# Performance work log

Hardware: AMD Instinct MI355X
Metric: run time of the kernel (lower is better)

Reference implementation:

```python
import jax, jax.numpy as jnp
import numpy as np

B, N, D, H, DK, DV = 16, 512, 512, 8, 64, 64


def setup_inputs() -> dict:
    key = jax.random.key(0)
    ks = jax.random.split(key, 16)
    xav = lambda k, fi, fo: jax.random.uniform(k, (fi, fo), jnp.float32,
                                               -jnp.sqrt(6.0 / (fi + fo)), jnp.sqrt(6.0 / (fi + fo)))
    return {
        "queries": jax.random.normal(ks[0], (B, N, D), jnp.float32),
        "keys": jax.random.normal(ks[1], (B, N, D), jnp.float32),
        "values": jax.random.normal(ks[2], (B, N, D), jnp.float32),
        "box_relation_embed_matrix": jax.random.uniform(ks[3], (B, H, N, N), jnp.float32),
        "ExtrAtt": jax.random.normal(ks[4], (B, H, N, N), jnp.float32),
        "Wq": xav(ks[5], D, H * DK), "bq": jnp.zeros((H * DK,), jnp.float32),
        "Wk": xav(ks[6], D, H * DK), "bk": jnp.zeros((H * DK,), jnp.float32),
        "Wv": xav(ks[7], D, H * DV), "bv": jnp.zeros((H * DV,), jnp.float32),
        "Wo": xav(ks[8], H * DV, D), "bo": jnp.zeros((D,), jnp.float32),
    }


def reference(queries, keys, values, box_relation_embed_matrix, ExtrAtt,
              Wq, bq, Wk, bk, Wv, bv, Wo, bo):
    b_s, nq, _ = queries.shape
    nk = keys.shape[1]
    # projections -> [B, H, N, d]
    q = (queries @ Wq + bq).reshape(b_s, nq, H, DK).transpose(0, 2, 1, 3)
    k = (keys @ Wk + bk).reshape(b_s, nk, H, DK).transpose(0, 2, 1, 3)
    v = (values @ Wv + bv).reshape(b_s, nk, H, DV).transpose(0, 2, 1, 3)
    scale = 1.0 / jnp.sqrt(jnp.asarray(DK, queries.dtype))
    att = jnp.einsum('bhqd,bhkd->bhqk', q, k) * scale
    # log geometric (box) bias + content attention, first softmax
    w_mn = jnp.log(jnp.clip(box_relation_embed_matrix, 1e-6, None)) + att
    w_mn = jax.nn.softmax(w_mn, axis=-1)
    # dropout is identity in eval; add extra attention and re-normalize
    att2 = jax.nn.softmax(w_mn + ExtrAtt, axis=-1)
    out = jnp.einsum('bhqk,bhkd->bhqd', att2, v)
    out = out.transpose(0, 2, 1, 3).reshape(b_s, nq, H * DV)
    return out @ Wo + bo
```

## Files before the change

kernel.cpp:

```cpp
#include <hip/hip_runtime.h>
#include <hip/hip_bf16.h>

#define NB 16
#define NN 512
#define ND 512
#define NH 8

using short8 = __attribute__((ext_vector_type(8))) short;
using f32x4  = __attribute__((ext_vector_type(4))) float;

static __device__ __forceinline__ unsigned short f2bf(float f) {
  unsigned u = __builtin_bit_cast(unsigned, f);
  unsigned r = 0x7fffu + ((u >> 16) & 1u);
  return (unsigned short)((u + r) >> 16);
}

__global__ __launch_bounds__(256) void wprep(
    const float* __restrict__ Wq, const float* __restrict__ Wk,
    const float* __restrict__ Wv, const float* __restrict__ Wo,
    unsigned short* __restrict__ T) {
  const float* W;
  switch (blockIdx.z) {
    case 0: W = Wq; break;
    case 1: W = Wk; break;
    case 2: W = Wv; break;
    default: W = Wo; break;
  }
  unsigned short* Wt = T + (size_t)blockIdx.z * 512 * 512;
  __shared__ float tile[64][65];
  const int t = threadIdx.x;
  const int k0 = blockIdx.x * 64, n0 = blockIdx.y * 64;
#pragma unroll
  for (int it = 0; it < 4; ++it) {
    int row = it * 16 + (t >> 4);
    int c4 = (t & 15) * 4;
    float4 v = *(const float4*)&W[(size_t)(k0 + row) * 512 + n0 + c4];
    tile[row][c4] = v.x; tile[row][c4 + 1] = v.y;
    tile[row][c4 + 2] = v.z; tile[row][c4 + 3] = v.w;
  }
  __syncthreads();
#pragma unroll
  for (int it = 0; it < 4; ++it) {
    int nr = it * 16 + (t >> 4);
    int k4 = (t & 15) * 4;
    ushort4 o;
    o.x = f2bf(tile[k4 + 0][nr]); o.y = f2bf(tile[k4 + 1][nr]);
    o.z = f2bf(tile[k4 + 2][nr]); o.w = f2bf(tile[k4 + 3][nr]);
    *(ushort4*)&Wt[(size_t)(n0 + nr) * 512 + k0 + k4] = o;
  }
}

__global__ __launch_bounds__(256) void qkv_gemm(
    const float* __restrict__ Xq, const float* __restrict__ Xk,
    const float* __restrict__ Xv, const unsigned short* __restrict__ Wt,
    const float* __restrict__ bq, const float* __restrict__ bk,
    const float* __restrict__ bv, unsigned short* __restrict__ q_ws,
    unsigned short* __restrict__ k_ws, unsigned short* __restrict__ vt_ws) {
  const int zi = blockIdx.z;
  const float* X = (zi == 0) ? Xq : (zi == 1) ? Xk : Xv;
  const unsigned short* Wz = Wt + (size_t)zi * 512 * 512;
  const float* bias = (zi == 0) ? bq : (zi == 1) ? bk : bv;
  const int m0 = blockIdx.x * 128, n0 = blockIdx.y * 128;
  __shared__ unsigned short Al[2][128][40];
  __shared__ unsigned short Bl[2][128][40];
  const int t = threadIdx.x;
  const int w = t >> 6, l = t & 63;
  const int lr = l & 15, lg = l >> 4;
  const int wr = (w >> 1) * 64, wc = (w & 1) * 64;
  f32x4 acc[4][4] = {};
  for (int kk = 0; kk < 512; kk += 64) {
    __syncthreads();
    {
      const int colk = (t & 15) * 4;
      const int kc = colk >> 5, kin = colk & 31;
#pragma unroll
      for (int p = 0; p < 8; ++p) {
        int row = p * 16 + (t >> 4);
        float4 v = *(const float4*)&X[(size_t)(m0 + row) * 512 + kk + colk];
        ushort4 o;
        o.x = f2bf(v.x); o.y = f2bf(v.y); o.z = f2bf(v.z); o.w = f2bf(v.w);
        *(ushort4*)&Al[kc][row][kin] = o;
      }
      const int colk8 = (t & 7) * 8;
      const int kc2 = colk8 >> 5, kin2 = colk8 & 31;
#pragma unroll
      for (int p = 0; p < 4; ++p) {
        int row = p * 32 + (t >> 3);
        short8 v = *(const short8*)&Wz[(size_t)(n0 + row) * 512 + kk + colk8];
        *(short8*)&Bl[kc2][row][kin2] = v;
      }
    }
    __syncthreads();
#pragma unroll
    for (int kc = 0; kc < 2; ++kc) {
      short8 a[4], b[4];
      const int lk = lg * 8;
#pragma unroll
      for (int i = 0; i < 4; ++i) a[i] = *(const short8*)&Al[kc][wr + i * 16 + lr][lk];
#pragma unroll
      for (int i = 0; i < 4; ++i) b[i] = *(const short8*)&Bl[kc][wc + i * 16 + lr][lk];
#pragma unroll
      for (int i = 0; i < 4; ++i)
#pragma unroll
        for (int j = 0; j < 4; ++j)
          acc[i][j] = __builtin_amdgcn_mfma_f32_16x16x32_bf16(a[i], b[j], acc[i][j], 0, 0, 0);
    }
  }
#pragma unroll
  for (int j = 0; j < 4; ++j) {
    const int col = n0 + wc + j * 16 + lr;
    const float bb = bias[col];
    const int hh = col >> 6, dv = col & 63;
#pragma unroll
    for (int i = 0; i < 4; ++i) {
      const int mbase = m0 + wr + i * 16 + lg * 4;
      const int b_ = mbase >> 9, nt = mbase & 511;
      if (zi == 2) {
        ushort4 o;
        o.x = f2bf(acc[i][j][0] + bb); o.y = f2bf(acc[i][j][1] + bb);
        o.z = f2bf(acc[i][j][2] + bb); o.w = f2bf(acc[i][j][3] + bb);
        *(ushort4*)&vt_ws[((size_t)(b_ * NH + hh) * 64 + dv) * 512 + nt] = o;
      } else {
        unsigned short* dst = (zi == 0) ? q_ws : k_ws;
#pragma unroll
        for (int r = 0; r < 4; ++r)
          dst[((size_t)(b_ * NH + hh) * 512 + nt + r) * 64 + dv] = f2bf(acc[i][j][r] + bb);
      }
    }
  }
}

__global__ __launch_bounds__(256, 3) void attn_kernel(
    const unsigned short* __restrict__ q_ws, const unsigned short* __restrict__ k_ws,
    const unsigned short* __restrict__ vt_ws, const float* __restrict__ box,
    const float* __restrict__ Ext, unsigned short* __restrict__ hidden) {
  const int t = threadIdx.x;
  const int w = t >> 6, l = t & 63;
  const int lr = l & 15, lg = l >> 4;
  const int bh = blockIdx.y;
  const int q0 = blockIdx.x * 32;
  const int b = bh >> 3, h = bh & 7;

  const unsigned short* Qp = q_ws + (size_t)bh * 512 * 64;
  const unsigned short* Kp = k_ws + (size_t)bh * 512 * 64;
  const unsigned short* Vt = vt_ws + (size_t)bh * 64 * 512;
  const float* boxp = box + ((size_t)bh * 512 + q0) * 512;
  const float* Ep = Ext + ((size_t)bh * 512 + q0) * 512;

  __shared__ float red[4][32];
  __shared__ float red2[4][32];
  __shared__ __align__(16) unsigned char wsh[4][9216];

  const int n0w = w * 128;

  f32x4 bx[2][8];
#pragma unroll
  for (int c = 0; c < 8; ++c) {
    const int cb = n0w + c * 16 + lg * 4;
    bx[0][c] = *(const f32x4*)&boxp[(size_t)lr * 512 + cb];
    bx[1][c] = *(const f32x4*)&boxp[(size_t)(16 + lr) * 512 + cb];
  }
  __builtin_amdgcn_sched_barrier(0);

  short8 qf[2][2];
#pragma unroll
  for (int rg = 0; rg < 2; ++rg)
#pragma unroll
    for (int kc = 0; kc < 2; ++kc)
      qf[rg][kc] = *(const short8*)&Qp[(size_t)(q0 + rg * 16 + lr) * 64 + kc * 32 + lg * 8];

  f32x4 z[2][8];
  float s1a = 0.f, s1b = 0.f;
#pragma unroll
  for (int c = 0; c < 8; ++c) {
    const int krow = n0w + c * 16 + lr;
    short8 kf0 = *(const short8*)&Kp[(size_t)krow * 64 + lg * 8];
    short8 kf1 = *(const short8*)&Kp[(size_t)krow * 64 + 32 + lg * 8];
    f32x4 a0 = {0.f, 0.f, 0.f, 0.f}, a1 = {0.f, 0.f, 0.f, 0.f};
    a0 = __builtin_amdgcn_mfma_f32_16x16x32_bf16(kf0, qf[0][0], a0, 0, 0, 0);
    a0 = __builtin_amdgcn_mfma_f32_16x16x32_bf16(kf1, qf[0][1], a0, 0, 0, 0);
    a1 = __builtin_amdgcn_mfma_f32_16x16x32_bf16(kf0, qf[1][0], a1, 0, 0, 0);
    a1 = __builtin_amdgcn_mfma_f32_16x16x32_bf16(kf1, qf[1][1], a1, 0, 0, 0);
#pragma unroll
    for (int r = 0; r < 4; ++r) {
      float e0 = __expf(a0[r] * 0.125f + __logf(fmaxf(bx[0][c][r], 1e-6f)));
      float e1 = __expf(a1[r] * 0.125f + __logf(fmaxf(bx[1][c][r], 1e-6f)));
      z[0][c][r] = e0; s1a += e0;
      z[1][c][r] = e1; s1b += e1;
    }
  }
  s1a += __shfl_xor(s1a, 16); s1a += __shfl_xor(s1a, 32);
  s1b += __shfl_xor(s1b, 16); s1b += __shfl_xor(s1b, 32);
  if (lg == 0) {
    red[w][lr] = s1a;
    red[w][16 + lr] = s1b;
  }
  f32x4 ex[2][8];
#pragma unroll
  for (int c = 0; c < 8; ++c) {
    const int cb = n0w + c * 16 + lg * 4;
    ex[0][c] = *(const f32x4*)&Ep[(size_t)lr * 512 + cb];
    ex[1][c] = *(const f32x4*)&Ep[(size_t)(16 + lr) * 512 + cb];
  }
  __builtin_amdgcn_sched_barrier(0);
  __syncthreads();
  float l1i[2];
#pragma unroll
  for (int rg = 0; rg < 2; ++rg) {
    const int lrow = rg * 16 + lr;
    l1i[rg] = 1.0f / (red[0][lrow] + red[1][lrow] + red[2][lrow] + red[3][lrow]);
  }
  float s2a = 0.f, s2b = 0.f;
#pragma unroll
  for (int c = 0; c < 8; ++c)
#pragma unroll
    for (int r = 0; r < 4; ++r) {
      float e0 = __expf(z[0][c][r] * l1i[0] + ex[0][c][r]);
      float e1 = __expf(z[1][c][r] * l1i[1] + ex[1][c][r]);
      z[0][c][r] = e0; s2a += e0;
      z[1][c][r] = e1; s2b += e1;
    }
  s2a += __shfl_xor(s2a, 16); s2a += __shfl_xor(s2a, 32);
  s2b += __shfl_xor(s2b, 16); s2b += __shfl_xor(s2b, 32);
  if (lg == 0) {
    red2[w][lr] = s2a;
    red2[w][16 + lr] = s2b;
  }
  __syncthreads();
  float l2i[2];
#pragma unroll
  for (int rg = 0; rg < 2; ++rg) {
    const int lrow = rg * 16 + lr;
    l2i[rg] = 1.0f / (red2[0][lrow] + red2[1][lrow] + red2[2][lrow] + red2[3][lrow]);
  }
  unsigned short(*Pw)[144] = (unsigned short(*)[144])wsh[w];
#pragma unroll
  for (int rg = 0; rg < 2; ++rg)
#pragma unroll
    for (int c = 0; c < 8; ++c) {
      ushort4 o;
      o.x = f2bf(z[rg][c][0] * l2i[rg]);
      o.y = f2bf(z[rg][c][1] * l2i[rg]);
      o.z = f2bf(z[rg][c][2] * l2i[rg]);
      o.w = f2bf(z[rg][c][3] * l2i[rg]);
      *(ushort4*)&Pw[rg * 16 + lr][c * 16 + lg * 4] = o;
    }
  f32x4 o[2][4] = {};
#pragma unroll
  for (int kc = 0; kc < 4; ++kc) {
    short8 pa0 = *(const short8*)&Pw[lr][kc * 32 + lg * 8];
    short8 pa1 = *(const short8*)&Pw[16 + lr][kc * 32 + lg * 8];
#pragma unroll
    for (int c2 = 0; c2 < 4; ++c2) {
      short8 vf = *(const short8*)&Vt[(size_t)(c2 * 16 + lr) * 512 + n0w + kc * 32 + lg * 8];
      o[0][c2] = __builtin_amdgcn_mfma_f32_16x16x32_bf16(pa0, vf, o[0][c2], 0, 0, 0);
      o[1][c2] = __builtin_amdgcn_mfma_f32_16x16x32_bf16(pa1, vf, o[1][c2], 0, 0, 0);
    }
  }
  float* ow = (float*)wsh[w];
#pragma unroll
  for (int rg = 0; rg < 2; ++rg)
#pragma unroll
    for (int c2 = 0; c2 < 4; ++c2)
#pragma unroll
      for (int r = 0; r < 4; ++r)
        ow[(rg * 16 + lg * 4 + r) * 68 + c2 * 16 + lr] = o[rg][c2][r];
  __syncthreads();
#pragma unroll
  for (int i = 0; i < 2; ++i) {
    const int lrow = i * 16 + (t >> 4);
    const int d4 = (t & 15) * 4;
    f32x4 s = *(const f32x4*)&((const float*)wsh[0])[lrow * 68 + d4];
#pragma unroll
    for (int w2 = 1; w2 < 4; ++w2) {
      f32x4 p = *(const f32x4*)&((const float*)wsh[w2])[lrow * 68 + d4];
#pragma unroll
      for (int r = 0; r < 4; ++r) s[r] += p[r];
    }
    ushort4 oo;
    oo.x = f2bf(s[0]); oo.y = f2bf(s[1]); oo.z = f2bf(s[2]); oo.w = f2bf(s[3]);
    *(ushort4*)&hidden[(size_t)(b * 512 + q0 + lrow) * 512 + h * 64 + d4] = oo;
  }
}

__global__ __launch_bounds__(256) void out_gemm(
    const unsigned short* __restrict__ hidden, const unsigned short* __restrict__ WoT,
    const float* __restrict__ bo, float* __restrict__ out) {
  const int m0 = blockIdx.x * 128, n0 = blockIdx.y * 128;
  __shared__ unsigned short Al[2][128][40];
  __shared__ unsigned short Bl[2][128][40];
  const int t = threadIdx.x;
  const int w = t >> 6, l = t & 63;
  const int lr = l & 15, lg = l >> 4;
  const int wr = (w >> 1) * 64, wc = (w & 1) * 64;
  f32x4 acc[4][4] = {};
  for (int kk = 0; kk < 512; kk += 64) {
    __syncthreads();
    {
      const int colk8 = (t & 7) * 8;
      const int kc2 = colk8 >> 5, kin2 = colk8 & 31;
#pragma unroll
      for (int p = 0; p < 4; ++p) {
        int row = p * 32 + (t >> 3);
        short8 v = *(const short8*)&hidden[(size_t)(m0 + row) * 512 + kk + colk8];
        *(short8*)&Al[kc2][row][kin2] = v;
      }
#pragma unroll
      for (int p = 0; p < 4; ++p) {
        int row = p * 32 + (t >> 3);
        short8 v = *(const short8*)&WoT[(size_t)(n0 + row) * 512 + kk + colk8];
        *(short8*)&Bl[kc2][row][kin2] = v;
      }
    }
    __syncthreads();
#pragma unroll
    for (int kc = 0; kc < 2; ++kc) {
      short8 a[4], b[4];
      const int lk = lg * 8;
#pragma unroll
      for (int i = 0; i < 4; ++i) a[i] = *(const short8*)&Al[kc][wr + i * 16 + lr][lk];
#pragma unroll
      for (int i = 0; i < 4; ++i) b[i] = *(const short8*)&Bl[kc][wc + i * 16 + lr][lk];
#pragma unroll
      for (int i = 0; i < 4; ++i)
#pragma unroll
        for (int j = 0; j < 4; ++j)
          acc[i][j] = __builtin_amdgcn_mfma_f32_16x16x32_bf16(a[i], b[j], acc[i][j], 0, 0, 0);
    }
  }
#pragma unroll
  for (int j = 0; j < 4; ++j) {
    const int col = n0 + wc + j * 16 + lr;
    const float bb = bo[col];
#pragma unroll
    for (int i = 0; i < 4; ++i)
#pragma unroll
      for (int r = 0; r < 4; ++r)
        out[(size_t)(m0 + wr + i * 16 + lg * 4 + r) * 512 + col] = acc[i][j][r] + bb;
  }
}

extern "C" void kernel_launch(void* const* d_in, const int* in_sizes, int n_in,
                              void* d_out, int out_size, void* d_ws, size_t ws_size,
                              hipStream_t stream) {
  const float* queries = (const float*)d_in[0];
  const float* keys = (const float*)d_in[1];
  const float* values = (const float*)d_in[2];
  const float* box = (const float*)d_in[3];
  const float* ext = (const float*)d_in[4];
  const float* Wq = (const float*)d_in[5];
  const float* bq = (const float*)d_in[6];
  const float* Wk = (const float*)d_in[7];
  const float* bk = (const float*)d_in[8];
  const float* Wv = (const float*)d_in[9];
  const float* bv = (const float*)d_in[10];
  const float* Wo = (const float*)d_in[11];
  const float* bo = (const float*)d_in[12];
  float* out = (float*)d_out;

  char* ws = (char*)d_ws;
  unsigned short* q_ws = (unsigned short*)(ws);
  unsigned short* k_ws = (unsigned short*)(ws + 8u * 1024 * 1024);
  unsigned short* vt_ws = (unsigned short*)(ws + 16u * 1024 * 1024);
  unsigned short* hidden = (unsigned short*)(ws + 24u * 1024 * 1024);
  unsigned short* wt = (unsigned short*)(ws + 32u * 1024 * 1024);

  wprep<<<dim3(8, 8, 4), 256, 0, stream>>>(Wq, Wk, Wv, Wo, wt);
  qkv_gemm<<<dim3(64, 4, 3), 256, 0, stream>>>(queries, keys, values, wt, bq, bk, bv,
                                               q_ws, k_ws, vt_ws);
  attn_kernel<<<dim3(16, 128), 256, 0, stream>>>(q_ws, k_ws, vt_ws, box, ext, hidden);
  out_gemm<<<dim3(64, 4), 256, 0, stream>>>(hidden, wt + 3u * 512 * 512, bo, out);
}
```

Before: 146.7 us.

## Halve attention query tile, stage probabilities in LDS, raise occupancy

The attention kernel now handles 16 query rows per block instead of 32 and launches twice as many blocks with a launch bound of 8 blocks per CU. Intermediate softmax values are kept as bf16 in shared memory rather than in large register arrays. log(box)+exp is replaced by box*exp(att), and the second normalization is applied after the PV matmul. The aim is to cut register pressure so more waves can hide the latency of the large box/ExtrAtt fp32 streams. In exchange, the first-softmax numerators are rounded to bf16 before the second exp, which adds precision risk, and each block reloads K/V for fewer queries.

```diff
diff --git a/kernel.cpp b/kernel.cpp
--- a/kernel.cpp
+++ b/kernel.cpp
@@ -13,6 +13,9 @@
   unsigned u = __builtin_bit_cast(unsigned, f);
   unsigned r = 0x7fffu + ((u >> 16) & 1u);
   return (unsigned short)((u + r) >> 16);
+}
+static __device__ __forceinline__ float bf2f(unsigned short u) {
+  return __builtin_bit_cast(float, (unsigned)u << 16);
 }
 
 __global__ __launch_bounds__(256) void wprep(
@@ -130,7 +133,7 @@
   }
 }
 
-__global__ __launch_bounds__(256, 3) void attn_kernel(
+__global__ __launch_bounds__(256, 8) void attn_kernel(
     const unsigned short* __restrict__ q_ws, const unsigned short* __restrict__ k_ws,
     const unsigned short* __restrict__ vt_ws, const float* __restrict__ box,
     const float* __restrict__ Ext, unsigned short* __restrict__ hidden) {
@@ -138,7 +141,7 @@
   const int w = t >> 6, l = t & 63;
   const int lr = l & 15, lg = l >> 4;
   const int bh = blockIdx.y;
-  const int q0 = blockIdx.x * 32;
+  const int q0 = blockIdx.x * 16;
   const int b = bh >> 3, h = bh & 7;
 
   const unsigned short* Qp = q_ws + (size_t)bh * 512 * 64;
@@ -147,128 +150,93 @@
   const float* boxp = box + ((size_t)bh * 512 + q0) * 512;
   const float* Ep = Ext + ((size_t)bh * 512 + q0) * 512;
 
-  __shared__ float red[4][32];
-  __shared__ float red2[4][32];
-  __shared__ __align__(16) unsigned char wsh[4][9216];
+  __shared__ float red[4][16];
+  __shared__ float red2[4][16];
+  __shared__ __align__(16) unsigned char wsh[4][4352];
 
   const int n0w = w * 128;
-
-  f32x4 bx[2][8];
-#pragma unroll
-  for (int c = 0; c < 8; ++c) {
-    const int cb = n0w + c * 16 + lg * 4;
-    bx[0][c] = *(const f32x4*)&boxp[(size_t)lr * 512 + cb];
-    bx[1][c] = *(const f32x4*)&boxp[(size_t)(16 + lr) * 512 + cb];
-  }
-  __builtin_amdgcn_sched_barrier(0);
-
-  short8 qf[2][2];
-#pragma unroll
-  for (int rg = 0; rg < 2; ++rg)
-#pragma unroll
-    for (int kc = 0; kc < 2; ++kc)
-      qf[rg][kc] = *(const short8*)&Qp[(size_t)(q0 + rg * 16 + lr) * 64 + kc * 32 + lg * 8];
-
-  f32x4 z[2][8];
-  float s1a = 0.f, s1b = 0.f;
+  unsigned short(*Pw)[136] = (unsigned short(*)[136])wsh[w];
+
+  short8 qf0 = *(const short8*)&Qp[(size_t)(q0 + lr) * 64 + lg * 8];
+  short8 qf1 = *(const short8*)&Qp[(size_t)(q0 + lr) * 64 + 32 + lg * 8];
+
+  float s1 = 0.f;
 #pragma unroll
   for (int c = 0; c < 8; ++c) {
     const int krow = n0w + c * 16 + lr;
     short8 kf0 = *(const short8*)&Kp[(size_t)krow * 64 + lg * 8];
     short8 kf1 = *(const short8*)&Kp[(size_t)krow * 64 + 32 + lg * 8];
-    f32x4 a0 = {0.f, 0.f, 0.f, 0.f}, a1 = {0.f, 0.f, 0.f, 0.f};
-    a0 = __builtin_amdgcn_mfma_f32_16x16x32_bf16(kf0, qf[0][0], a0, 0, 0, 0);
-    a0 = __builtin_amdgcn_mfma_f32_16x16x32_bf16(kf1, qf[0][1], a0, 0, 0, 0);
-    a1 = __builtin_amdgcn_mfma_f32_16x16x32_bf16(kf0, qf[1][0], a1, 0, 0, 0);
-    a1 = __builtin_amdgcn_mfma_f32_16x16x32_bf16(kf1, qf[1][1], a1, 0, 0, 0);
-#pragma unroll
-    for (int r = 0; r < 4; ++r) {
-      float e0 = __expf(a0[r] * 0.125f + __logf(fmaxf(bx[0][c][r], 1e-6f)));
-      float e1 = __expf(a1[r] * 0.125f + __logf(fmaxf(bx[1][c][r], 1e-6f)));
-      z[0][c][r] = e0; s1a += e0;
-      z[1][c][r] = e1; s1b += e1;
-    }
-  }
-  s1a += __shfl_xor(s1a, 16); s1a += __shfl_xor(s1a, 32);
-  s1b += __shfl_xor(s1b, 16); s1b += __shfl_xor(s1b, 32);
-  if (lg == 0) {
-    red[w][lr] = s1a;
-    red[w][16 + lr] = s1b;
-  }
-  f32x4 ex[2][8];
+    f32x4 bx4 = *(const f32x4*)&boxp[(size_t)lr * 512 + n0w + c * 16 + lg * 4];
+    f32x4 a = {0.f, 0.f, 0.f, 0.f};
+    a = __builtin_amdgcn_mfma_f32_16x16x32_bf16(kf0, qf0, a, 0, 0, 0);
+    a = __builtin_amdgcn_mfma_f32_16x16x32_bf16(kf1, qf1, a, 0, 0, 0);
+    ushort4 o;
+    {
+      float e0 = fmaxf(bx4[0], 1e-6f) * __expf(a[0] * 0.125f);
+      float e1 = fmaxf(bx4[1], 1e-6f) * __expf(a[1] * 0.125f);
+      float e2 = fmaxf(bx4[2], 1e-6f) * __expf(a[2] * 0.125f);
+      float e3 = fmaxf(bx4[3], 1e-6f) * __expf(a[3] * 0.125f);
+      s1 += (e0 + e1) + (e2 + e3);
+      o.x = f2bf(e0); o.y = f2bf(e1); o.z = f2bf(e2); o.w = f2bf(e3);
+    }
+    *(ushort4*)&Pw[lr][c * 16 + lg * 4] = o;
+  }
+  s1 += __shfl_xor(s1, 16);
+  s1 += __shfl_xor(s1, 32);
+  if (lg == 0) red[w][lr] = s1;
+  __syncthreads();
+  const float l1i = 1.0f / (red[0][lr] + red[1][lr] + red[2][lr] + red[3][lr]);
+
+  float s2 = 0.f;
 #pragma unroll
   for (int c = 0; c < 8; ++c) {
-    const int cb = n0w + c * 16 + lg * 4;
-    ex[0][c] = *(const f32x4*)&Ep[(size_t)lr * 512 + cb];
-    ex[1][c] = *(const f32x4*)&Ep[(size_t)(16 + lr) * 512 + cb];
-  }
-  __builtin_amdgcn_sched_barrier(0);
+    f32x4 ex4 = *(const f32x4*)&Ep[(size_t)lr * 512 + n0w + c * 16 + lg * 4];
+    ushort4 u = *(const ushort4*)&Pw[lr][c * 16 + lg * 4];
+    ushort4 o;
+    {
+      float e0 = __expf(bf2f(u.x) * l1i + ex4[0]);
+      float e1 = __expf(bf2f(u.y) * l1i + ex4[1]);
+      float e2 = __expf(bf2f(u.z) * l1i + ex4[2]);
+      float e3 = __expf(bf2f(u.w) * l1i + ex4[3]);
+      s2 += (e0 + e1) + (e2 + e3);
+      o.x = f2bf(e0); o.y = f2bf(e1); o.z = f2bf(e2); o.w = f2bf(e3);
+    }
+    *(ushort4*)&Pw[lr][c * 16 + lg * 4] = o;
+  }
+  s2 += __shfl_xor(s2, 16);
+  s2 += __shfl_xor(s2, 32);
+  if (lg == 0) red2[w][lr] = s2;
   __syncthreads();
-  float l1i[2];
-#pragma unroll
-  for (int rg = 0; rg < 2; ++rg) {
-    const int lrow = rg * 16 + lr;
-    l1i[rg] = 1.0f / (red[0][lrow] + red[1][lrow] + red[2][lrow] + red[3][lrow]);
-  }
-  float s2a = 0.f, s2b = 0.f;
-#pragma unroll
-  for (int c = 0; c < 8; ++c)
-#pragma unroll
-    for (int r = 0; r < 4; ++r) {
-      float e0 = __expf(z[0][c][r] * l1i[0] + ex[0][c][r]);
-      float e1 = __expf(z[1][c][r] * l1i[1] + ex[1][c][r]);
-      z[0][c][r] = e0; s2a += e0;
-      z[1][c][r] = e1; s2b += e1;
-    }
-  s2a += __shfl_xor(s2a, 16); s2a += __shfl_xor(s2a, 32);
-  s2b += __shfl_xor(s2b, 16); s2b += __shfl_xor(s2b, 32);
-  if (lg == 0) {
-    red2[w][lr] = s2a;
-    red2[w][16 + lr] = s2b;
-  }
-  __syncthreads();
-  float l2i[2];
-#pragma unroll
-  for (int rg = 0; rg < 2; ++rg) {
-    const int lrow = rg * 16 + lr;
-    l2i[rg] = 1.0f / (red2[0][lrow] + red2[1][lrow] + red2[2][lrow] + red2[3][lrow]);
-  }
-  unsigned short(*Pw)[144] = (unsigned short(*)[144])wsh[w];
-#pragma unroll
-  for (int rg = 0; rg < 2; ++rg)
-#pragma unroll
-    for (int c = 0; c < 8; ++c) {
-      ushort4 o;
-      o.x = f2bf(z[rg][c][0] * l2i[rg]);
-      o.y = f2bf(z[rg][c][1] * l2i[rg]);
-      o.z = f2bf(z[rg][c][2] * l2i[rg]);
-      o.w = f2bf(z[rg][c][3] * l2i[rg]);
-      *(ushort4*)&Pw[rg * 16 + lr][c * 16 + lg * 4] = o;
-    }
-  f32x4 o[2][4] = {};
+
+  f32x4 o4[4] = {};
 #pragma unroll
   for (int kc = 0; kc < 4; ++kc) {
-    short8 pa0 = *(const short8*)&Pw[lr][kc * 32 + lg * 8];
-    short8 pa1 = *(const short8*)&Pw[16 + lr][kc * 32 + lg * 8];
+    short8 pa = *(const short8*)&Pw[lr][kc * 32 + lg * 8];
 #pragma unroll
     for (int c2 = 0; c2 < 4; ++c2) {
       short8 vf = *(const short8*)&Vt[(size_t)(c2 * 16 + lr) * 512 + n0w + kc * 32 + lg * 8];
-      o[0][c2] = __builtin_amdgcn_mfma_f32_16x16x32_bf16(pa0, vf, o[0][c2], 0, 0, 0);
-      o[1][c2] = __builtin_amdgcn_mfma_f32_16x16x32_bf16(pa1, vf, o[1][c2], 0, 0, 0);
-    }
-  }
+      o4[c2] = __builtin_amdgcn_mfma_f32_16x16x32_bf16(pa, vf, o4[c2], 0, 0, 0);
+    }
+  }
+  f32x4 rs = *(const f32x4*)&red2[0][lg * 4];
+#pragma unroll
+  for (int w2 = 1; w2 < 4; ++w2) {
+    f32x4 p = *(const f32x4*)&red2[w2][lg * 4];
+#pragma unroll
+    for (int r = 0; r < 4; ++r) rs[r] += p[r];
+  }
+  f32x4 l2v;
+#pragma unroll
+  for (int r = 0; r < 4; ++r) l2v[r] = 1.0f / rs[r];
   float* ow = (float*)wsh[w];
 #pragma unroll
-  for (int rg = 0; rg < 2; ++rg)
-#pragma unroll
-    for (int c2 = 0; c2 < 4; ++c2)
-#pragma unroll
-      for (int r = 0; r < 4; ++r)
-        ow[(rg * 16 + lg * 4 + r) * 68 + c2 * 16 + lr] = o[rg][c2][r];
+  for (int c2 = 0; c2 < 4; ++c2)
+#pragma unroll
+    for (int r = 0; r < 4; ++r)
+      ow[(lg * 4 + r) * 68 + c2 * 16 + lr] = o4[c2][r] * l2v[r];
   __syncthreads();
-#pragma unroll
-  for (int i = 0; i < 2; ++i) {
-    const int lrow = i * 16 + (t >> 4);
+  {
+    const int lrow = t >> 4;
     const int d4 = (t & 15) * 4;
     f32x4 s = *(const f32x4*)&((const float*)wsh[0])[lrow * 68 + d4];
 #pragma unroll
@@ -368,6 +336,6 @@
   wprep<<<dim3(8, 8, 4), 256, 0, stream>>>(Wq, Wk, Wv, Wo, wt);
   qkv_gemm<<<dim3(64, 4, 3), 256, 0, stream>>>(queries, keys, values, wt, bq, bk, bv,
                                                q_ws, k_ws, vt_ws);
-  attn_kernel<<<dim3(16, 128), 256, 0, stream>>>(q_ws, k_ws, vt_ws, box, ext, hidden);
+  attn_kernel<<<dim3(32, 128), 256, 0, stream>>>(q_ws, k_ws, vt_ws, box, ext, hidden);
   out_gemm<<<dim3(64, 4), 256, 0, stream>>>(hidden, wt + 3u * 512 * 512, bo, out);
 }
```

After: 176.5 us. 1.2x slower.

## Process four query tiles per block with register-resident K and XCD-aware mapping

Applied to the files above, without the earlier changes.

The attention grid shrinks from 2048 blocks to 512, and each block now loops over four 32-row query tiles, keeping its K fragments in registers across the tiles. Block indices are remapped so that blocks sharing a batch-head land on the same XCD, improving L2 reuse of K and V. The log/exp of the box bias is replaced by multiplying the clamped box value with exp of the scaled score, which removes one transcendental per element. The trade-offs are fewer blocks to hide latency, higher register pressure from the cached K fragments, and the loss of the explicit sched_barrier prefetch ordering.

```diff
diff --git a/kernel.cpp b/kernel.cpp
--- a/kernel.cpp
+++ b/kernel.cpp
@@ -137,149 +137,159 @@
   const int t = threadIdx.x;
   const int w = t >> 6, l = t & 63;
   const int lr = l & 15, lg = l >> 4;
-  const int bh = blockIdx.y;
-  const int q0 = blockIdx.x * 32;
+  const int wg = blockIdx.x;
+  const int xcd = wg & 7, slot = wg >> 3;
+  const int bh = xcd + 8 * (slot >> 2);
+  const int qg = slot & 3;
   const int b = bh >> 3, h = bh & 7;
 
   const unsigned short* Qp = q_ws + (size_t)bh * 512 * 64;
   const unsigned short* Kp = k_ws + (size_t)bh * 512 * 64;
   const unsigned short* Vt = vt_ws + (size_t)bh * 64 * 512;
-  const float* boxp = box + ((size_t)bh * 512 + q0) * 512;
-  const float* Ep = Ext + ((size_t)bh * 512 + q0) * 512;
 
   __shared__ float red[4][32];
   __shared__ float red2[4][32];
   __shared__ __align__(16) unsigned char wsh[4][9216];
 
   const int n0w = w * 128;
-
-  f32x4 bx[2][8];
-#pragma unroll
-  for (int c = 0; c < 8; ++c) {
-    const int cb = n0w + c * 16 + lg * 4;
-    bx[0][c] = *(const f32x4*)&boxp[(size_t)lr * 512 + cb];
-    bx[1][c] = *(const f32x4*)&boxp[(size_t)(16 + lr) * 512 + cb];
-  }
-  __builtin_amdgcn_sched_barrier(0);
-
-  short8 qf[2][2];
-#pragma unroll
-  for (int rg = 0; rg < 2; ++rg)
-#pragma unroll
-    for (int kc = 0; kc < 2; ++kc)
-      qf[rg][kc] = *(const short8*)&Qp[(size_t)(q0 + rg * 16 + lr) * 64 + kc * 32 + lg * 8];
-
-  f32x4 z[2][8];
-  float s1a = 0.f, s1b = 0.f;
+  unsigned short(*Pw)[144] = (unsigned short(*)[144])wsh[w];
+
+  short8 kf[8][2];
 #pragma unroll
   for (int c = 0; c < 8; ++c) {
     const int krow = n0w + c * 16 + lr;
-    short8 kf0 = *(const short8*)&Kp[(size_t)krow * 64 + lg * 8];
-    short8 kf1 = *(const short8*)&Kp[(size_t)krow * 64 + 32 + lg * 8];
-    f32x4 a0 = {0.f, 0.f, 0.f, 0.f}, a1 = {0.f, 0.f, 0.f, 0.f};
-    a0 = __builtin_amdgcn_mfma_f32_16x16x32_bf16(kf0, qf[0][0], a0, 0, 0, 0);
-    a0 = __builtin_amdgcn_mfma_f32_16x16x32_bf16(kf1, qf[0][1], a0, 0, 0, 0);
-    a1 = __builtin_amdgcn_mfma_f32_16x16x32_bf16(kf0, qf[1][0], a1, 0, 0, 0);
-    a1 = __builtin_amdgcn_mfma_f32_16x16x32_bf16(kf1, qf[1][1], a1, 0, 0, 0);
-#pragma unroll
-    for (int r = 0; r < 4; ++r) {
-      float e0 = __expf(a0[r] * 0.125f + __logf(fmaxf(bx[0][c][r], 1e-6f)));
-      float e1 = __expf(a1[r] * 0.125f + __logf(fmaxf(bx[1][c][r], 1e-6f)));
-      z[0][c][r] = e0; s1a += e0;
-      z[1][c][r] = e1; s1b += e1;
-    }
-  }
-  s1a += __shfl_xor(s1a, 16); s1a += __shfl_xor(s1a, 32);
-  s1b += __shfl_xor(s1b, 16); s1b += __shfl_xor(s1b, 32);
-  if (lg == 0) {
-    red[w][lr] = s1a;
-    red[w][16 + lr] = s1b;
-  }
-  f32x4 ex[2][8];
-#pragma unroll
-  for (int c = 0; c < 8; ++c) {
-    const int cb = n0w + c * 16 + lg * 4;
-    ex[0][c] = *(const f32x4*)&Ep[(size_t)lr * 512 + cb];
-    ex[1][c] = *(const f32x4*)&Ep[(size_t)(16 + lr) * 512 + cb];
-  }
-  __builtin_amdgcn_sched_barrier(0);
-  __syncthreads();
-  float l1i[2];
-#pragma unroll
-  for (int rg = 0; rg < 2; ++rg) {
-    const int lrow = rg * 16 + lr;
-    l1i[rg] = 1.0f / (red[0][lrow] + red[1][lrow] + red[2][lrow] + red[3][lrow]);
-  }
-  float s2a = 0.f, s2b = 0.f;
-#pragma unroll
-  for (int c = 0; c < 8; ++c)
-#pragma unroll
-    for (int r = 0; r < 4; ++r) {
-      float e0 = __expf(z[0][c][r] * l1i[0] + ex[0][c][r]);
-      float e1 = __expf(z[1][c][r] * l1i[1] + ex[1][c][r]);
-      z[0][c][r] = e0; s2a += e0;
-      z[1][c][r] = e1; s2b += e1;
-    }
-  s2a += __shfl_xor(s2a, 16); s2a += __shfl_xor(s2a, 32);
-  s2b += __shfl_xor(s2b, 16); s2b += __shfl_xor(s2b, 32);
-  if (lg == 0) {
-    red2[w][lr] = s2a;
-    red2[w][16 + lr] = s2b;
-  }
-  __syncthreads();
-  float l2i[2];
-#pragma unroll
-  for (int rg = 0; rg < 2; ++rg) {
-    const int lrow = rg * 16 + lr;
-    l2i[rg] = 1.0f / (red2[0][lrow] + red2[1][lrow] + red2[2][lrow] + red2[3][lrow]);
-  }
-  unsigned short(*Pw)[144] = (unsigned short(*)[144])wsh[w];
-#pragma unroll
-  for (int rg = 0; rg < 2; ++rg)
+    kf[c][0] = *(const short8*)&Kp[(size_t)krow * 64 + lg * 8];
+    kf[c][1] = *(const short8*)&Kp[(size_t)krow * 64 + 32 + lg * 8];
+  }
+
+  for (int tile = 0; tile < 4; ++tile) {
+    const int q0 = qg * 128 + tile * 32;
+    const float* boxp = box + ((size_t)bh * 512 + q0) * 512;
+    const float* Ep = Ext + ((size_t)bh * 512 + q0) * 512;
+
+    f32x4 bx[2][8];
 #pragma unroll
     for (int c = 0; c < 8; ++c) {
-      ushort4 o;
-      o.x = f2bf(z[rg][c][0] * l2i[rg]);
-      o.y = f2bf(z[rg][c][1] * l2i[rg]);
-      o.z = f2bf(z[rg][c][2] * l2i[rg]);
-      o.w = f2bf(z[rg][c][3] * l2i[rg]);
-      *(ushort4*)&Pw[rg * 16 + lr][c * 16 + lg * 4] = o;
-    }
-  f32x4 o[2][4] = {};
-#pragma unroll
-  for (int kc = 0; kc < 4; ++kc) {
-    short8 pa0 = *(const short8*)&Pw[lr][kc * 32 + lg * 8];
-    short8 pa1 = *(const short8*)&Pw[16 + lr][kc * 32 + lg * 8];
-#pragma unroll
-    for (int c2 = 0; c2 < 4; ++c2) {
-      short8 vf = *(const short8*)&Vt[(size_t)(c2 * 16 + lr) * 512 + n0w + kc * 32 + lg * 8];
-      o[0][c2] = __builtin_amdgcn_mfma_f32_16x16x32_bf16(pa0, vf, o[0][c2], 0, 0, 0);
-      o[1][c2] = __builtin_amdgcn_mfma_f32_16x16x32_bf16(pa1, vf, o[1][c2], 0, 0, 0);
-    }
-  }
-  float* ow = (float*)wsh[w];
-#pragma unroll
-  for (int rg = 0; rg < 2; ++rg)
-#pragma unroll
-    for (int c2 = 0; c2 < 4; ++c2)
-#pragma unroll
-      for (int r = 0; r < 4; ++r)
-        ow[(rg * 16 + lg * 4 + r) * 68 + c2 * 16 + lr] = o[rg][c2][r];
-  __syncthreads();
-#pragma unroll
-  for (int i = 0; i < 2; ++i) {
-    const int lrow = i * 16 + (t >> 4);
-    const int d4 = (t & 15) * 4;
-    f32x4 s = *(const f32x4*)&((const float*)wsh[0])[lrow * 68 + d4];
-#pragma unroll
-    for (int w2 = 1; w2 < 4; ++w2) {
-      f32x4 p = *(const f32x4*)&((const float*)wsh[w2])[lrow * 68 + d4];
-#pragma unroll
-      for (int r = 0; r < 4; ++r) s[r] += p[r];
-    }
-    ushort4 oo;
-    oo.x = f2bf(s[0]); oo.y = f2bf(s[1]); oo.z = f2bf(s[2]); oo.w = f2bf(s[3]);
-    *(ushort4*)&hidden[(size_t)(b * 512 + q0 + lrow) * 512 + h * 64 + d4] = oo;
+      const int cb = n0w + c * 16 + lg * 4;
+      bx[0][c] = *(const f32x4*)&boxp[(size_t)lr * 512 + cb];
+      bx[1][c] = *(const f32x4*)&boxp[(size_t)(16 + lr) * 512 + cb];
+    }
+
+    short8 qf[2][2];
+#pragma unroll
+    for (int rg = 0; rg < 2; ++rg)
+#pragma unroll
+      for (int kc = 0; kc < 2; ++kc)
+        qf[rg][kc] = *(const short8*)&Qp[(size_t)(q0 + rg * 16 + lr) * 64 + kc * 32 + lg * 8];
+
+    f32x4 z[2][8];
+    float s1a = 0.f, s1b = 0.f;
+#pragma unroll
+    for (int c = 0; c < 8; ++c) {
+      f32x4 a0 = {0.f, 0.f, 0.f, 0.f}, a1 = {0.f, 0.f, 0.f, 0.f};
+      a0 = __builtin_amdgcn_mfma_f32_16x16x32_bf16(kf[c][0], qf[0][0], a0, 0, 0, 0);
+      a0 = __builtin_amdgcn_mfma_f32_16x16x32_bf16(kf[c][1], qf[0][1], a0, 0, 0, 0);
+      a1 = __builtin_amdgcn_mfma_f32_16x16x32_bf16(kf[c][0], qf[1][0], a1, 0, 0, 0);
+      a1 = __builtin_amdgcn_mfma_f32_16x16x32_bf16(kf[c][1], qf[1][1], a1, 0, 0, 0);
+#pragma unroll
+      for (int r = 0; r < 4; ++r) {
+        float e0 = fmaxf(bx[0][c][r], 1e-6f) * __expf(a0[r] * 0.125f);
+        float e1 = fmaxf(bx[1][c][r], 1e-6f) * __expf(a1[r] * 0.125f);
+        z[0][c][r] = e0; s1a += e0;
+        z[1][c][r] = e1; s1b += e1;
+      }
+    }
+    s1a += __shfl_xor(s1a, 16); s1a += __shfl_xor(s1a, 32);
+    s1b += __shfl_xor(s1b, 16); s1b += __shfl_xor(s1b, 32);
+    if (lg == 0) {
+      red[w][lr] = s1a;
+      red[w][16 + lr] = s1b;
+    }
+    f32x4 ex[2][8];
+#pragma unroll
+    for (int c = 0; c < 8; ++c) {
+      const int cb = n0w + c * 16 + lg * 4;
+      ex[0][c] = *(const f32x4*)&Ep[(size_t)lr * 512 + cb];
+      ex[1][c] = *(const f32x4*)&Ep[(size_t)(16 + lr) * 512 + cb];
+    }
+    __syncthreads();
+    float l1i[2];
+#pragma unroll
+    for (int rg = 0; rg < 2; ++rg) {
+      const int lrow = rg * 16 + lr;
+      l1i[rg] = 1.0f / (red[0][lrow] + red[1][lrow] + red[2][lrow] + red[3][lrow]);
+    }
+    float s2a = 0.f, s2b = 0.f;
+#pragma unroll
+    for (int c = 0; c < 8; ++c)
+#pragma unroll
+      for (int r = 0; r < 4; ++r) {
+        float e0 = __expf(z[0][c][r] * l1i[0] + ex[0][c][r]);
+        float e1 = __expf(z[1][c][r] * l1i[1] + ex[1][c][r]);
+        z[0][c][r] = e0; s2a += e0;
+        z[1][c][r] = e1; s2b += e1;
+      }
+    s2a += __shfl_xor(s2a, 16); s2a += __shfl_xor(s2a, 32);
+    s2b += __shfl_xor(s2b, 16); s2b += __shfl_xor(s2b, 32);
+    if (lg == 0) {
+      red2[w][lr] = s2a;
+      red2[w][16 + lr] = s2b;
+    }
+    __syncthreads();
+    float l2i[2];
+#pragma unroll
+    for (int rg = 0; rg < 2; ++rg) {
+      const int lrow = rg * 16 + lr;
+      l2i[rg] = 1.0f / (red2[0][lrow] + red2[1][lrow] + red2[2][lrow] + red2[3][lrow]);
+    }
+#pragma unroll
+    for (int rg = 0; rg < 2; ++rg)
+#pragma unroll
+      for (int c = 0; c < 8; ++c) {
+        ushort4 o;
+        o.x = f2bf(z[rg][c][0] * l2i[rg]);
+        o.y = f2bf(z[rg][c][1] * l2i[rg]);
+        o.z = f2bf(z[rg][c][2] * l2i[rg]);
+        o.w = f2bf(z[rg][c][3] * l2i[rg]);
+        *(ushort4*)&Pw[rg * 16 + lr][c * 16 + lg * 4] = o;
+      }
+    f32x4 o[2][4] = {};
+#pragma unroll
+    for (int kc = 0; kc < 4; ++kc) {
+      short8 pa0 = *(const short8*)&Pw[lr][kc * 32 + lg * 8];
+      short8 pa1 = *(const short8*)&Pw[16 + lr][kc * 32 + lg * 8];
+#pragma unroll
+      for (int c2 = 0; c2 < 4; ++c2) {
+        short8 vf = *(const short8*)&Vt[(size_t)(c2 * 16 + lr) * 512 + n0w + kc * 32 + lg * 8];
+        o[0][c2] = __builtin_amdgcn_mfma_f32_16x16x32_bf16(pa0, vf, o[0][c2], 0, 0, 0);
+        o[1][c2] = __builtin_amdgcn_mfma_f32_16x16x32_bf16(pa1, vf, o[1][c2], 0, 0, 0);
+      }
+    }
+    float* ow = (float*)wsh[w];
+#pragma unroll
+    for (int rg = 0; rg < 2; ++rg)
+#pragma unroll
+      for (int c2 = 0; c2 < 4; ++c2)
+#pragma unroll
+        for (int r = 0; r < 4; ++r)
+          ow[(rg * 16 + lg * 4 + r) * 68 + c2 * 16 + lr] = o[rg][c2][r];
+    __syncthreads();
+#pragma unroll
+    for (int i = 0; i < 2; ++i) {
+      const int lrow = i * 16 + (t >> 4);
+      const int d4 = (t & 15) * 4;
+      f32x4 s = *(const f32x4*)&((const float*)wsh[0])[lrow * 68 + d4];
+#pragma unroll
+      for (int w2 = 1; w2 < 4; ++w2) {
+        f32x4 p = *(const f32x4*)&((const float*)wsh[w2])[lrow * 68 + d4];
+#pragma unroll
+        for (int r = 0; r < 4; ++r) s[r] += p[r];
+      }
+      ushort4 oo;
+      oo.x = f2bf(s[0]); oo.y = f2bf(s[1]); oo.z = f2bf(s[2]); oo.w = f2bf(s[3]);
+      *(ushort4*)&hidden[(size_t)(b * 512 + q0 + lrow) * 512 + h * 64 + d4] = oo;
+    }
+    __syncthreads();
   }
 }
 
@@ -368,6 +378,6 @@
   wprep<<<dim3(8, 8, 4), 256, 0, stream>>>(Wq, Wk, Wv, Wo, wt);
   qkv_gemm<<<dim3(64, 4, 3), 256, 0, stream>>>(queries, keys, values, wt, bq, bk, bv,
                                                q_ws, k_ws, vt_ws);
-  attn_kernel<<<dim3(16, 128), 256, 0, stream>>>(q_ws, k_ws, vt_ws, box, ext, hidden);
+  attn_kernel<<<dim3(512), 256, 0, stream>>>(q_ws, k_ws, vt_ws, box, ext, hidden);
   out_gemm<<<dim3(64, 4), 256, 0, stream>>>(hidden, wt + 3u * 512 * 512, bo, out);
 }
```

Result: slower. 202.1 us (+37.7%).
